# Optimization experiments

Hardware: AMD Instinct MI355X
Metric: run time of the kernel (lower is better)

Reference implementation:

```python
import jax, jax.numpy as jnp
import numpy as np

H = 768      # hidden_size
R = 64       # lora_dim
E = 8        # n_experts
B, S = 8, 2048


def setup_inputs() -> dict:
    key = jax.random.key(0)
    ks = jax.random.split(key, 10)
    s_in = 1.0 / np.sqrt(H)
    s_r = 1.0 / np.sqrt(R)
    return {
        "x": jax.random.normal(ks[0], (B, S, H), dtype=jnp.float32),
        "enc_w": jax.random.uniform(ks[1], (H, R), jnp.float32, -s_in, s_in),
        "enc_b": jax.random.uniform(ks[2], (R,), jnp.float32, -s_in, s_in),
        "sw_w": jax.random.uniform(ks[3], (R, E), jnp.float32, -s_r, s_r),
        "sw_b": jax.random.uniform(ks[4], (E,), jnp.float32, -s_r, s_r),
        "w1": jax.random.uniform(ks[5], (E, H, R), jnp.float32, -s_in, s_in),
        "b1": jax.random.uniform(ks[6], (E, R), jnp.float32, -s_in, s_in),
        "w2": jax.random.uniform(ks[7], (E, R, H), jnp.float32, -s_r, s_r),
        "b2": jax.random.uniform(ks[8], (E, H), jnp.float32, -s_r, s_r),
    }


def reference(x, enc_w, enc_b, sw_w, sw_b, w1, b1, w2, b2):
    b, s, d = x.shape
    xt = x.reshape(-1, d)                                  # [T, H]
    # router: encoder -> switch -> softmax -> top-1
    x_enc = xt @ enc_w + enc_b                             # [T, R]
    route_prob = jax.nn.softmax(x_enc @ sw_w + sw_b, axis=-1)  # [T, E]
    route_prob_max = jnp.max(route_prob, axis=-1)          # [T]
    routes = jnp.argmax(route_prob, axis=-1)               # [T]
    onehot = jax.nn.one_hot(routes, E, dtype=xt.dtype)     # [T, E]
    # dense dispatch: per-(token, expert) LoRA bottleneck; masked combine
    h = jnp.einsum('td,edr->ter', xt, w1) + b1[None]       # [T, E, R]
    h = jax.nn.gelu(h, approximate=False)
    h = h * onehot[..., None]                              # zero non-routed
    out = jnp.einsum('ter,erd->td', h, w2) + onehot @ b2   # [T, H]
    out = out * route_prob_max[:, None]
    return out.reshape(b, s, d)
```

## Files before the change

### kernel.cpp

```cpp
#include <hip/hip_runtime.h>
#include <math.h>

#define HDIM 768
#define RDIM 64
#define NEXP 8
#define NTOK 16384

typedef _Float16 half8 __attribute__((ext_vector_type(8)));
typedef float float4_t __attribute__((ext_vector_type(4)));

__device__ __forceinline__ float gelu_exact(float v) {
    return 0.5f * v * (1.0f + erff(v * 0.70710678118654752440f));
}

__global__ __launch_bounds__(256) void prep_kernel(
    const float* __restrict__ w1, const float* __restrict__ w2,
    const float* __restrict__ enc_w, const float* __restrict__ enc_b,
    const float* __restrict__ sw_w, const float* __restrict__ sw_b,
    _Float16* __restrict__ w1t, _Float16* __restrict__ w2t,
    float* __restrict__ wrt, float* __restrict__ brr)
{
    const int wid = blockIdx.x * 4 + (threadIdx.x >> 6);
    const int lane = threadIdx.x & 63;
    if (wid < 768) {
        const int e = wid / 96, k0 = (wid % 96) * 8;
        half8 o;
        #pragma unroll
        for (int j = 0; j < 8; j++)
            o[j] = (_Float16)w1[((size_t)(e * HDIM + k0 + j)) * RDIM + lane];
        *(half8*)(w1t + ((size_t)(e * RDIM + lane)) * HDIM + k0) = o;
    } else if (wid < 1536) {
        const int id = wid - 768;
        const int e = id / 96, rem = id % 96;
        const int n = (rem >> 3) * 64 + lane, k0 = (rem & 7) * 8;
        half8 o;
        #pragma unroll
        for (int j = 0; j < 8; j++)
            o[j] = (_Float16)w2[((size_t)(e * RDIM + k0 + j)) * HDIM + n];
        *(half8*)(w2t + ((size_t)(e * HDIM + n)) * RDIM + k0) = o;
    } else if (wid < 1632) {
        const int k = (wid - 1536) * 8 + (lane >> 3);
        const int e = lane & 7;
        float s = 0.0f;
        #pragma unroll 16
        for (int r = 0; r < RDIM; r++)
            s += enc_w[(size_t)k * RDIM + r] * sw_w[r * NEXP + e];
        wrt[e * HDIM + k] = s;
    } else if (wid == 1632) {
        if (lane < NEXP) {
            float s = sw_b[lane];
            #pragma unroll 16
            for (int r = 0; r < RDIM; r++)
                s += enc_b[r] * sw_w[r * NEXP + lane];
            brr[lane] = s;
        }
    }
}

__global__ __launch_bounds__(256, 4) void router_kernel(
    const float* __restrict__ x, const float* __restrict__ wrt,
    const float* __restrict__ brr, float* __restrict__ pmax,
    int* __restrict__ counts, int* __restrict__ lists)
{
    __shared__ __align__(16) float wrl[NEXP][772];
    __shared__ int lcnt[NEXP], gbase[NEXP];

    const int tid = threadIdx.x;
    #pragma unroll
    for (int i0 = 0; i0 < 6; i0++) {
        const int i = tid + i0 * 256;
        const int e = i / 192, k4 = (i % 192) * 4;
        *(float4*)&wrl[e][k4] = *(const float4*)(wrt + e * HDIM + k4);
    }
    if (tid < NEXP) lcnt[tid] = 0;

    const int wv = tid >> 6, lane = tid & 63;
    const int h = lane & 31, hw = lane >> 5;

    float br[8];
    #pragma unroll
    for (int e = 0; e < 8; e++) br[e] = brr[e];
    __syncthreads();

    int amv[2], lpv[2], tkv[2];
    #pragma unroll
    for (int it = 0; it < 2; it++) {
        const int tok = blockIdx.x * 16 + it * 8 + wv * 2 + hw;
        const float* xrow = x + (size_t)tok * HDIM;
        float4 xv[6];
        #pragma unroll
        for (int g = 0; g < 6; g++)
            xv[g] = *(const float4*)(xrow + g * 128 + h * 4);

        float acc[8];
        #pragma unroll
        for (int e = 0; e < 8; e++) acc[e] = 0.0f;
        #pragma unroll
        for (int e = 0; e < 8; e++) {
            #pragma unroll
            for (int g = 0; g < 6; g++) {
                const float4 w4 = *(const float4*)&wrl[e][g * 128 + h * 4];
                acc[e] = fmaf(xv[g].x, w4.x, acc[e]);
                acc[e] = fmaf(xv[g].y, w4.y, acc[e]);
                acc[e] = fmaf(xv[g].z, w4.z, acc[e]);
                acc[e] = fmaf(xv[g].w, w4.w, acc[e]);
            }
        }
        #pragma unroll
        for (int d = 1; d < 32; d <<= 1) {
            #pragma unroll
            for (int e = 0; e < 8; e++)
                acc[e] += __shfl_xor(acc[e], d);
        }
        float lg[8];
        lg[0] = acc[0] + br[0];
        float m = lg[0]; int am = 0;
        #pragma unroll
        for (int e = 1; e < 8; e++) {
            lg[e] = acc[e] + br[e];
            if (lg[e] > m) { m = lg[e]; am = e; }
        }
        float s = 0.0f;
        #pragma unroll
        for (int e = 0; e < 8; e++) s += expf(lg[e] - m);

        amv[it] = -1;
        if (h == 0) {
            pmax[tok] = 1.0f / s;
            amv[it] = am;
            lpv[it] = atomicAdd(&lcnt[am], 1);
            tkv[it] = tok;
        }
    }
    __syncthreads();
    if (tid < NEXP) gbase[tid] = atomicAdd(&counts[tid * 32], lcnt[tid]);
    __syncthreads();
    #pragma unroll
    for (int it = 0; it < 2; it++)
        if (amv[it] >= 0)
            lists[amv[it] * NTOK + gbase[amv[it]] + lpv[it]] = tkv[it];
}

__global__ __launch_bounds__(256, 4) void mm12_kernel(
    const float* __restrict__ x, const _Float16* __restrict__ w1t,
    const float* __restrict__ b1, const _Float16* __restrict__ w2t,
    const float* __restrict__ b2, const float* __restrict__ pmax,
    const int* __restrict__ counts, const int* __restrict__ lists,
    float* __restrict__ out)
{
    __shared__ __align__(16) _Float16 xt[16][776];
    __shared__ __align__(16) _Float16 hl[16][72];
    __shared__ float pml[16];
    __shared__ int tkl[16];

    const int e = blockIdx.x;
    const int cnt = counts[e * 32];
    const int tid = threadIdx.x;
    const int wv = tid >> 6, lane = tid & 63;
    const int q = lane >> 4, c = lane & 15;

    for (int st = blockIdx.y; st * 16 < cnt; st += gridDim.y) {
        const int base = st * 16;
        const int nt = cnt - base;

        if (tid < 16) {
            const int t = lists[e * NTOK + base + min(tid, nt - 1)];
            tkl[tid] = t;
            pml[tid] = pmax[t];
        }

        #pragma unroll
        for (int rr = 0; rr < 4; rr++) {
            const int row = wv * 4 + rr;
            const int tok = lists[e * NTOK + base + min(row, nt - 1)];
            const float* xr = x + (size_t)tok * HDIM;
            #pragma unroll
            for (int j = 0; j < 3; j++) {
                float4 v = *(const float4*)(xr + j * 256 + lane * 4);
                union { _Float16 hv[4]; unsigned long long u; } pk;
                pk.hv[0] = (_Float16)v.x; pk.hv[1] = (_Float16)v.y;
                pk.hv[2] = (_Float16)v.z; pk.hv[3] = (_Float16)v.w;
                *(unsigned long long*)&xt[row][j * 256 + lane * 4] = pk.u;
            }
        }
        __syncthreads();

        {
            const _Float16* wbase =
                w1t + ((size_t)(e * RDIM + wv * 16 + c)) * HDIM + q * 8;
            float4_t acc = {0, 0, 0, 0};
            #pragma unroll 6
            for (int k0 = 0; k0 < HDIM; k0 += 32) {
                half8 a = *(const half8*)&xt[c][k0 + q * 8];
                half8 b = *(const half8*)(wbase + k0);
                acc = __builtin_amdgcn_mfma_f32_16x16x32_f16(a, b, acc, 0, 0, 0);
            }
            const float b1v = b1[e * RDIM + wv * 16 + c];
            #pragma unroll
            for (int i = 0; i < 4; i++)
                hl[q * 4 + i][wv * 16 + c] = (_Float16)gelu_exact(acc[i] + b1v);
        }
        __syncthreads();

        {
            half8 a0 = *(const half8*)&hl[c][q * 8];
            half8 a1 = *(const half8*)&hl[c][32 + q * 8];
            int tokv[4]; float pm[4]; bool ok[4];
            #pragma unroll
            for (int i = 0; i < 4; i++) {
                const int row = q * 4 + i;
                ok[i] = row < nt;
                tokv[i] = tkl[row];
                pm[i] = pml[row];
            }
            #pragma unroll 4
            for (int nf = 0; nf < 12; nf++) {
                const int n = wv * 192 + nf * 16 + c;
                const _Float16* wrow = w2t + ((size_t)(e * HDIM + n)) * RDIM;
                half8 b0  = *(const half8*)(wrow + q * 8);
                half8 b1h = *(const half8*)(wrow + 32 + q * 8);
                float4_t acc2 = {0, 0, 0, 0};
                acc2 = __builtin_amdgcn_mfma_f32_16x16x32_f16(a0, b0, acc2, 0, 0, 0);
                acc2 = __builtin_amdgcn_mfma_f32_16x16x32_f16(a1, b1h, acc2, 0, 0, 0);
                const float b2v = b2[e * HDIM + n];
                #pragma unroll
                for (int i = 0; i < 4; i++) {
                    if (ok[i])
                        out[(size_t)tokv[i] * HDIM + n] = (acc2[i] + b2v) * pm[i];
                }
            }
        }
        __syncthreads();
    }
}

extern "C" void kernel_launch(void* const* d_in, const int* in_sizes, int n_in,
                              void* d_out, int out_size, void* d_ws, size_t ws_size,
                              hipStream_t stream) {
    const float* x     = (const float*)d_in[0];
    const float* enc_w = (const float*)d_in[1];
    const float* enc_b = (const float*)d_in[2];
    const float* sw_w  = (const float*)d_in[3];
    const float* sw_b  = (const float*)d_in[4];
    const float* w1    = (const float*)d_in[5];
    const float* b1    = (const float*)d_in[6];
    const float* w2    = (const float*)d_in[7];
    const float* b2    = (const float*)d_in[8];
    float* out = (float*)d_out;

    char* p = (char*)d_ws;
    int*      counts = (int*)p;
    float*    pmax   = (float*)(p + 1024);
    int*      lists  = (int*)(p + 66560);
    float*    wrt    = (float*)(p + 590848);
    float*    brr    = (float*)(p + 615424);
    _Float16* w1t    = (_Float16*)(p + 615680);
    _Float16* w2t    = (_Float16*)(p + 1402112);

    hipMemsetAsync(d_ws, 0, 1024, stream);

    hipLaunchKernelGGL(prep_kernel, dim3(409), dim3(256), 0, stream,
                       w1, w2, enc_w, enc_b, sw_w, sw_b, w1t, w2t, wrt, brr);
    hipLaunchKernelGGL(router_kernel, dim3(NTOK / 16), dim3(256), 0, stream,
                       x, wrt, brr, pmax, counts, lists);
    hipLaunchKernelGGL(mm12_kernel, dim3(NEXP, 128), dim3(256), 0, stream,
                       x, w1t, b1, w2t, b2, pmax, counts, lists, out);
}
```

Baseline: 184.9 us.

## Software-pipeline x gathers in mm12 with register prefetch and double-buffered LDS

New measurement: 196.8 us. 1.06x slower.

```diff
diff --git a/kernel.cpp b/kernel.cpp
--- a/kernel.cpp
+++ b/kernel.cpp
@@ -141,17 +141,17 @@
             lists[amv[it] * NTOK + gbase[amv[it]] + lpv[it]] = tkv[it];
 }
 
-__global__ __launch_bounds__(256, 4) void mm12_kernel(
+__global__ __launch_bounds__(256, 3) void mm12_kernel(
     const float* __restrict__ x, const _Float16* __restrict__ w1t,
     const float* __restrict__ b1, const _Float16* __restrict__ w2t,
     const float* __restrict__ b2, const float* __restrict__ pmax,
     const int* __restrict__ counts, const int* __restrict__ lists,
     float* __restrict__ out)
 {
-    __shared__ __align__(16) _Float16 xt[16][776];
+    __shared__ __align__(16) _Float16 xt[2][16][776];
     __shared__ __align__(16) _Float16 hl[16][72];
-    __shared__ float pml[16];
-    __shared__ int tkl[16];
+    __shared__ float pml[2][16];
+    __shared__ int tkl[2][16];
 
     const int e = blockIdx.x;
     const int cnt = counts[e * 32];
@@ -159,31 +159,62 @@
     const int wv = tid >> 6, lane = tid & 63;
     const int q = lane >> 4, c = lane & 15;
 
-    for (int st = blockIdx.y; st * 16 < cnt; st += gridDim.y) {
+    int st = blockIdx.y;
+    if (st * 16 >= cnt) return;
+
+    float4 xv[12];
+    {
         const int base = st * 16;
         const int nt = cnt - base;
-
-        if (tid < 16) {
-            const int t = lists[e * NTOK + base + min(tid, nt - 1)];
-            tkl[tid] = t;
-            pml[tid] = pmax[t];
-        }
-
         #pragma unroll
         for (int rr = 0; rr < 4; rr++) {
             const int row = wv * 4 + rr;
             const int tok = lists[e * NTOK + base + min(row, nt - 1)];
             const float* xr = x + (size_t)tok * HDIM;
             #pragma unroll
+            for (int j = 0; j < 3; j++)
+                xv[rr * 3 + j] = *(const float4*)(xr + j * 256 + lane * 4);
+        }
+    }
+
+    int buf = 0;
+    while (st * 16 < cnt) {
+        const int base = st * 16;
+        const int nt = cnt - base;
+
+        if (tid < 16) {
+            const int t = lists[e * NTOK + base + min(tid, nt - 1)];
+            tkl[buf][tid] = t;
+            pml[buf][tid] = pmax[t];
+        }
+        #pragma unroll
+        for (int rr = 0; rr < 4; rr++) {
+            const int row = wv * 4 + rr;
+            #pragma unroll
             for (int j = 0; j < 3; j++) {
-                float4 v = *(const float4*)(xr + j * 256 + lane * 4);
+                float4 v = xv[rr * 3 + j];
                 union { _Float16 hv[4]; unsigned long long u; } pk;
                 pk.hv[0] = (_Float16)v.x; pk.hv[1] = (_Float16)v.y;
                 pk.hv[2] = (_Float16)v.z; pk.hv[3] = (_Float16)v.w;
-                *(unsigned long long*)&xt[row][j * 256 + lane * 4] = pk.u;
+                *(unsigned long long*)&xt[buf][row][j * 256 + lane * 4] = pk.u;
             }
         }
         __syncthreads();
+
+        const int nst = st + gridDim.y;
+        if (nst * 16 < cnt) {
+            const int nbase = nst * 16;
+            const int nnt = cnt - nbase;
+            #pragma unroll
+            for (int rr = 0; rr < 4; rr++) {
+                const int row = wv * 4 + rr;
+                const int tok = lists[e * NTOK + nbase + min(row, nnt - 1)];
+                const float* xr = x + (size_t)tok * HDIM;
+                #pragma unroll
+                for (int j = 0; j < 3; j++)
+                    xv[rr * 3 + j] = *(const float4*)(xr + j * 256 + lane * 4);
+            }
+        }
 
         {
             const _Float16* wbase =
@@ -191,7 +222,7 @@
             float4_t acc = {0, 0, 0, 0};
             #pragma unroll 6
             for (int k0 = 0; k0 < HDIM; k0 += 32) {
-                half8 a = *(const half8*)&xt[c][k0 + q * 8];
+                half8 a = *(const half8*)&xt[buf][c][k0 + q * 8];
                 half8 b = *(const half8*)(wbase + k0);
                 acc = __builtin_amdgcn_mfma_f32_16x16x32_f16(a, b, acc, 0, 0, 0);
             }
@@ -210,8 +241,8 @@
             for (int i = 0; i < 4; i++) {
                 const int row = q * 4 + i;
                 ok[i] = row < nt;
-                tokv[i] = tkl[row];
-                pm[i] = pml[row];
+                tokv[i] = tkl[buf][row];
+                pm[i] = pml[buf][row];
             }
             #pragma unroll 4
             for (int nf = 0; nf < 12; nf++) {
@@ -230,7 +261,7 @@
                 }
             }
         }
-        __syncthreads();
+        st = nst; buf ^= 1;
     }
 }
 
@@ -263,6 +294,6 @@
                        w1, w2, enc_w, enc_b, sw_w, sw_b, w1t, w2t, wrt, brr);
     hipLaunchKernelGGL(router_kernel, dim3(NTOK / 16), dim3(256), 0, stream,
                        x, wrt, brr, pmax, counts, lists);
-    hipLaunchKernelGGL(mm12_kernel, dim3(NEXP, 128), dim3(256), 0, stream,
+    hipLaunchKernelGGL(mm12_kernel, dim3(NEXP, 64), dim3(256), 0, stream,
                        x, w1t, b1, w2t, b2, pmax, counts, lists, out);
 }
```
